# Performance work log

Measured on AMD Instinct MI355X. Metric: run time of the kernel, lower is better.

Reference implementation:

```python
import jax, jax.numpy as jnp
import numpy as np

# Tsit5 (Tsitouras 5(4)) Butcher tableau. 5th-order solution weights b == a7 row (FSAL).
A21 = 0.161
A31, A32 = -0.008480655492356989, 0.335480655492357
A41, A42, A43 = 2.8971530571054935, -6.359448489975075, 4.3622954328695815
A51, A52, A53, A54 = 5.325864828439257, -11.748883564062828, 7.4955393428898365, -0.09249506636175525
A61, A62, A63, A64, A65 = 5.86145544294642, -12.92096931784711, 8.159367898576159, -0.071584973281401, -0.028269050394068383
B1, B2, B3, B4, B5, B6 = 0.09646076681806523, 0.01, 0.4798896504144996, 1.379008574103742, -3.290069515436081, 2.324710524099774

B_TRAJ, D_STATE, D_FORCE, WIDTH = 1024, 256, 256, 512
T0, T1 = 0.0, 1.0
N_STEPS = 60  # fixed step h = DT0*SECOND = 60/3600 = 1/60 hour
H = (T1 - T0) / N_STEPS


def setup_inputs() -> dict:
    key = jax.random.key(0)
    ks = jax.random.split(key, 8)
    din = D_STATE + D_FORCE
    x0 = jax.random.normal(ks[0], (B_TRAJ, D_STATE), jnp.float32)
    u_forced = jax.random.normal(ks[1], (B_TRAJ, D_FORCE), jnp.float32) * 0.1
    W1 = jax.random.normal(ks[2], (WIDTH, din), jnp.float32) / np.sqrt(din)
    b1 = jnp.zeros((WIDTH,), jnp.float32)
    W2 = jax.random.normal(ks[3], (WIDTH, WIDTH), jnp.float32) / np.sqrt(WIDTH)
    b2 = jnp.zeros((WIDTH,), jnp.float32)
    W3 = jax.random.normal(ks[4], (D_STATE, WIDTH), jnp.float32) / np.sqrt(WIDTH)
    b3 = jnp.zeros((D_STATE,), jnp.float32)
    return dict(x0=x0, u_forced=u_forced, W1=W1, b1=b1, W2=W2, b2=b2, W3=W3, b3=b3)


def reference(x0, u_forced, W1, b1, W2, b2, W3, b3):
    # Augmented system: branch 0 = forced trajectory, branch 1 = unforced (zero force).
    # y: (2, B, D_STATE); u: (2, B, D_FORCE)
    y0 = jnp.stack([x0, x0])
    u = jnp.stack([u_forced, jnp.zeros_like(u_forced)])

    def mlp(z):  # z: (2, B, din) -> (2, B, D_STATE); eqx.nn.MLP default relu
        h = jax.nn.relu(jnp.einsum('kbi,oi->kbo', z, W1) + b1)
        h = jax.nn.relu(jnp.einsum('kbi,oi->kbo', h, W2) + b2)
        return jnp.einsum('kbi,oi->kbo', h, W3) + b3

    def f(y):  # ForcedVectorField: mlp(hstack((x, u))) on both branches at once
        return mlp(jnp.concatenate([y, u], axis=-1))

    def tsit5_step(y, _):
        k1 = f(y)
        k2 = f(y + H * (A21 * k1))
        k3 = f(y + H * (A31 * k1 + A32 * k2))
        k4 = f(y + H * (A41 * k1 + A42 * k2 + A43 * k3))
        k5 = f(y + H * (A51 * k1 + A52 * k2 + A53 * k3 + A54 * k4))
        k6 = f(y + H * (A61 * k1 + A62 * k2 + A63 * k3 + A64 * k4 + A65 * k5))
        y_new = y + H * (B1 * k1 + B2 * k2 + B3 * k3 + B4 * k4 + B5 * k5 + B6 * k6)
        return y_new, None

    y_final, _ = jax.lax.scan(jax.checkpoint(tsit5_step), y0, None, length=N_STEPS)
    # (forced_state, unforced_state) at t1, stacked: (2, B, D_STATE)
    return y_final
```

## Files before the change

### kernel.cpp

```cpp
#include <hip/hip_runtime.h>
#include <hip/hip_bf16.h>

typedef short  short8  __attribute__((ext_vector_type(8)));
typedef float  float4v __attribute__((ext_vector_type(4)));

#define NSTEPS 60

constexpr double Hd = 1.0 / 60.0;
constexpr float HA1[1] = { (float)(Hd * 0.161) };
constexpr float HA2[2] = { (float)(Hd * -0.008480655492356989), (float)(Hd * 0.335480655492357) };
constexpr float HA3[3] = { (float)(Hd * 2.8971530571054935), (float)(Hd * -6.359448489975075),
                           (float)(Hd * 4.3622954328695815) };
constexpr float HA4[4] = { (float)(Hd * 5.325864828439257), (float)(Hd * -11.748883564062828),
                           (float)(Hd * 7.4955393428898365), (float)(Hd * -0.09249506636175525) };
constexpr float HA5[5] = { (float)(Hd * 5.86145544294642), (float)(Hd * -12.92096931784711),
                           (float)(Hd * 8.159367898576159), (float)(Hd * -0.071584973281401),
                           (float)(Hd * -0.028269050394068383) };
constexpr float HB6[6] = { (float)(Hd * 0.09646076681806523), (float)(Hd * 0.01),
                           (float)(Hd * 0.4798896504144996), (float)(Hd * 1.379008574103742),
                           (float)(Hd * -3.290069515436081), (float)(Hd * 2.324710524099774) };

__device__ __forceinline__ unsigned short f2bf(float f) {
    union { float f; unsigned u; } v; v.f = f;
    unsigned r = v.u + 0x7fffu + ((v.u >> 16) & 1u);
    return (unsigned short)(r >> 16);
}

__global__ void wconv(const float* __restrict__ W1, const float* __restrict__ W2,
                      const float* __restrict__ W3, unsigned short* __restrict__ ws) {
    int g = blockIdx.x * blockDim.x + threadIdx.x;
    int blk = g >> 6, l = g & 63;
    const float* src;
    if (blk < 256) {
        int b = blk; int nt = b >> 3, ks = b & 7;
        int n = nt * 16 + (l & 15), k = ks * 32 + (l >> 4) * 8;
        src = W1 + n * 512 + k;
    } else if (blk < 768) {
        int b = blk - 256; int nt = b >> 4, ks = b & 15;
        int n = nt * 16 + (l & 15), k = ks * 32 + (l >> 4) * 8;
        src = W2 + n * 512 + k;
    } else {
        int b = blk - 768; int nt = b >> 4, ks = b & 15;
        int n = nt * 16 + (l & 15), k = ks * 32 + (l >> 4) * 8;
        src = W3 + n * 512 + k;
    }
    short8 v;
#pragma unroll
    for (int j = 0; j < 8; ++j) v[j] = (short)f2bf(src[j]);
    *(((short8*)ws) + g) = v;
}

template<int KDIM, int NT>
__device__ __forceinline__ void mfma_block(const unsigned short* __restrict__ lds, int stride,
                                           const short8* __restrict__ wb, int ntg0, int lane,
                                           float4v* acc) {
    const int row  = lane & 15;
    const int koff = (lane >> 4) * 8;
    const int rm   = (row & 7) << 3;
#pragma unroll
    for (int ks = 0; ks < KDIM / 32; ++ks) {
        const int nidx = ks * 32 + koff;
        short8 a = *(const short8*)(lds + row * stride + (nidx ^ rm));
#pragma unroll
        for (int nt = 0; nt < NT; ++nt) {
            short8 b = wb[(size_t)((ntg0 + nt) * (KDIM / 32) + ks) * 64 + lane];
            acc[nt] = __builtin_amdgcn_mfma_f32_16x16x32_bf16(a, b, acc[nt], 0, 0, 0);
        }
    }
}

__global__ void __launch_bounds__(512, 2) odeint(
        const float* __restrict__ x0, const float* __restrict__ uf,
        const float* __restrict__ W1, const float* __restrict__ b1,
        const float* __restrict__ b2, const float* __restrict__ b3,
        const unsigned short* __restrict__ ws, float* __restrict__ out) {
    __shared__ unsigned short xb[16 * 256];
    __shared__ unsigned short hb[16 * 512];
    __shared__ float c1s[8 * 512];
    __shared__ float bias2[512];
    __shared__ float bias3[256];

    const int tid  = threadIdx.x;
    const int wave = tid >> 6, lane = tid & 63;
    const int r0   = blockIdx.x * 8;

    float* utmp = (float*)hb;
    for (int i = tid; i < 8 * 256; i += 512) {
        int row = i >> 8, k = i & 255;
        int g = r0 + row;
        utmp[i] = (g < 1024) ? uf[g * 256 + k] : 0.f;
    }
    bias2[tid] = b2[tid];
    if (tid < 256) bias3[tid] = b3[tid];
    __syncthreads();

    {
        int n = tid;
        float acc8[8];
#pragma unroll
        for (int r = 0; r < 8; ++r) acc8[r] = b1[n];
        const float* wrow = W1 + n * 512 + 256;
        for (int k = 0; k < 256; ++k) {
            float w = wrow[k];
#pragma unroll
            for (int r = 0; r < 8; ++r) acc8[r] += w * utmp[r * 256 + k];
        }
#pragma unroll
        for (int r = 0; r < 8; ++r) c1s[r * 512 + n] = acc8[r];
    }
    __syncthreads();

    float ybr[8];
    float kreg[6][8];
    if (lane < 32) {
#pragma unroll
        for (int e = 0; e < 8; ++e) {
            int nt = e >> 2, r = e & 3;
            int row = (lane >> 4) * 4 + r;
            int n   = (wave * 2 + nt) * 16 + (lane & 15);
            int g   = r0 + row;
            ybr[e] = x0[(g & 1023) * 256 + n];
        }
    }

    const short8* wy1 = (const short8*)ws;
    const short8* w2  = (const short8*)(ws + 131072);
    const short8* w3  = (const short8*)(ws + 393216);

#define DO_STAGE(S, COEF) do {                                                          \
    if (lane < 32) {                                                                    \
        _Pragma("unroll")                                                               \
        for (int e = 0; e < 8; ++e) {                                                   \
            int nt_ = e >> 2, r_ = e & 3;                                               \
            int row_ = (lane >> 4) * 4 + r_;                                            \
            int n_   = (wave * 2 + nt_) * 16 + (lane & 15);                             \
            float v_ = ybr[e];                                                          \
            _Pragma("unroll")                                                           \
            for (int j = 0; j < S; ++j) v_ += COEF[j] * kreg[j][e];                     \
            xb[row_ * 256 + (n_ ^ ((row_ & 7) << 3))] = f2bf(v_);                       \
        }                                                                               \
    }                                                                                   \
    __syncthreads();             \
    {                                      \
        float4v a1[4];                                                                  \
        _Pragma("unroll") for (int q = 0; q < 4; ++q) a1[q] = (float4v){0.f,0.f,0.f,0.f}; \
        mfma_block<256, 4>(xb, 256, wy1, wave * 4, lane, a1);                           \
        if (lane < 32) {                                                                \
            _Pragma("unroll")                                                           \
            for (int nt = 0; nt < 4; ++nt) {                                            \
                int n_g = (wave * 4 + nt) * 16 + (lane & 15);                           \
                _Pragma("unroll")                                                       \
                for (int r = 0; r < 4; ++r) {                                           \
                    int row = (lane >> 4) * 4 + r;                                      \
                    float v = a1[nt][r] + c1s[row * 512 + n_g];                         \
                    v = fmaxf(v, 0.f);                                                  \
                    hb[row * 512 + (n_g ^ ((row & 7) << 3))] = f2bf(v);                 \
                }                                                                       \
            }                                                                           \
        }                                                                               \
    }                                                                                   \
    __syncthreads();                                                   \
    {          \
        float4v a2[4];                                                                  \
        _Pragma("unroll") for (int q = 0; q < 4; ++q) a2[q] = (float4v){0.f,0.f,0.f,0.f}; \
        mfma_block<512, 4>(hb, 512, w2, wave * 4, lane, a2);                            \
        __syncthreads();                                   \
        if (lane < 32) {                                                                \
            _Pragma("unroll")                                                           \
            for (int nt = 0; nt < 4; ++nt) {                                            \
                int n_g = (wave * 4 + nt) * 16 + (lane & 15);                           \
                _Pragma("unroll")                                                       \
                for (int r = 0; r < 4; ++r) {                                           \
                    int row = (lane >> 4) * 4 + r;                                      \
                    float v = a2[nt][r] + bias2[n_g];                                   \
                    v = fmaxf(v, 0.f);                                                  \
                    hb[row * 512 + (n_g ^ ((row & 7) << 3))] = f2bf(v);                 \
                }                                                                       \
            }                                                                           \
        }                                                                               \
    }                                                                                   \
    __syncthreads();                                                   \
    {        \
        float4v a3[2];                                                                  \
        _Pragma("unroll") for (int q = 0; q < 2; ++q) a3[q] = (float4v){0.f,0.f,0.f,0.f}; \
        mfma_block<512, 2>(hb, 512, w3, wave * 2, lane, a3);                            \
        if (lane < 32) {                                                                \
            _Pragma("unroll")                                                           \
            for (int nt = 0; nt < 2; ++nt) {                                            \
                int n_g = (wave * 2 + nt) * 16 + (lane & 15);                           \
                _Pragma("unroll")                                                       \
                for (int r = 0; r < 4; ++r) {                                           \
                    kreg[S][nt * 4 + r] = a3[nt][r] + bias3[n_g];                       \
                }                                                                       \
            }                                                                           \
        }                                                                               \
    }                                                                                   \
} while (0)

    for (int step = 0; step < NSTEPS; ++step) {
        DO_STAGE(0, HA1);
        DO_STAGE(1, HA1);
        DO_STAGE(2, HA2);
        DO_STAGE(3, HA3);
        DO_STAGE(4, HA4);
        DO_STAGE(5, HA5);
        if (lane < 32) {
#pragma unroll
            for (int e = 0; e < 8; ++e) {
                float v = ybr[e];
#pragma unroll
                for (int j = 0; j < 6; ++j) v += HB6[j] * kreg[j][e];
                ybr[e] = v;
            }
        }
    }
#undef DO_STAGE

    if (lane < 32) {
#pragma unroll
        for (int e = 0; e < 8; ++e) {
            int nt = e >> 2, r = e & 3;
            int row = (lane >> 4) * 4 + r;
            int n   = (wave * 2 + nt) * 16 + (lane & 15);
            out[(r0 + row) * 256 + n] = ybr[e];
        }
    }
}

extern "C" void kernel_launch(void* const* d_in, const int* in_sizes, int n_in,
                              void* d_out, int out_size, void* d_ws, size_t ws_size,
                              hipStream_t stream) {
    const float* x0 = (const float*)d_in[0];
    const float* uf = (const float*)d_in[1];
    const float* W1 = (const float*)d_in[2];
    const float* b1 = (const float*)d_in[3];
    const float* W2 = (const float*)d_in[4];
    const float* b2 = (const float*)d_in[5];
    const float* W3 = (const float*)d_in[6];
    const float* b3 = (const float*)d_in[7];
    unsigned short* ws = (unsigned short*)d_ws;

    wconv<<<128, 512, 0, stream>>>(W1, W2, W3, ws);
    odeint<<<256, 512, 0, stream>>>(x0, uf, W1, b1, b2, b3, ws, (float*)d_out);
}
```

Measured before the change: 14.98 ms.

## Process 16 real rows per block and prefetch MFMA operands

Each block now fills all 16 rows of the MFMA tile with real trajectories instead of 8, halving the grid to 128 blocks and removing wasted padded-row compute and duplicated weight streaming. The MFMA inner loop software-prefetches the next A/B fragments, and separate h1/h2 LDS buffers remove one barrier per stage. This trades fewer active blocks (half the CUs idle, one block per CU) and higher LDS use for less redundant work.

```diff
diff --git a/kernel.cpp b/kernel.cpp
--- a/kernel.cpp
+++ b/kernel.cpp
@@ -5,6 +5,9 @@
 typedef float  float4v __attribute__((ext_vector_type(4)));
 
 #define NSTEPS 60
+#define ROWS   16
+#define GRID   128
+#define C1S    518
 
 constexpr double Hd = 1.0 / 60.0;
 constexpr float HA1[1] = { (float)(Hd * 0.161) };
@@ -54,41 +57,59 @@
 __device__ __forceinline__ void mfma_block(const unsigned short* __restrict__ lds, int stride,
                                            const short8* __restrict__ wb, int ntg0, int lane,
                                            float4v* acc) {
+    constexpr int KS = KDIM / 32;
     const int row  = lane & 15;
     const int koff = (lane >> 4) * 8;
     const int rm   = (row & 7) << 3;
-#pragma unroll
-    for (int ks = 0; ks < KDIM / 32; ++ks) {
-        const int nidx = ks * 32 + koff;
-        short8 a = *(const short8*)(lds + row * stride + (nidx ^ rm));
-#pragma unroll
-        for (int nt = 0; nt < NT; ++nt) {
-            short8 b = wb[(size_t)((ntg0 + nt) * (KDIM / 32) + ks) * 64 + lane];
-            acc[nt] = __builtin_amdgcn_mfma_f32_16x16x32_bf16(a, b, acc[nt], 0, 0, 0);
-        }
-    }
-}
-
-__global__ void __launch_bounds__(512, 2) odeint(
+    const short8* wp = wb + (size_t)ntg0 * KS * 64 + lane;
+    short8 a_cur = *(const short8*)(lds + row * stride + (koff ^ rm));
+    short8 b_cur[NT];
+#pragma unroll
+    for (int nt = 0; nt < NT; ++nt) b_cur[nt] = wp[(size_t)nt * KS * 64];
+#pragma unroll
+    for (int ks = 0; ks < KS; ++ks) {
+        short8 a_nxt;
+        short8 b_nxt[NT];
+        if (ks + 1 < KS) {
+            a_nxt = *(const short8*)(lds + row * stride + (((ks + 1) * 32 + koff) ^ rm));
+#pragma unroll
+            for (int nt = 0; nt < NT; ++nt) b_nxt[nt] = wp[((size_t)nt * KS + ks + 1) * 64];
+        }
+#pragma unroll
+        for (int nt = 0; nt < NT; ++nt)
+            acc[nt] = __builtin_amdgcn_mfma_f32_16x16x32_bf16(a_cur, b_cur[nt], acc[nt], 0, 0, 0);
+        a_cur = a_nxt;
+#pragma unroll
+        for (int nt = 0; nt < NT; ++nt) b_cur[nt] = b_nxt[nt];
+    }
+}
+
+__global__ void __launch_bounds__(512, 1) odeint(
         const float* __restrict__ x0, const float* __restrict__ uf,
         const float* __restrict__ W1, const float* __restrict__ b1,
         const float* __restrict__ b2, const float* __restrict__ b3,
         const unsigned short* __restrict__ ws, float* __restrict__ out) {
     __shared__ unsigned short xb[16 * 256];
-    __shared__ unsigned short hb[16 * 512];
-    __shared__ float c1s[8 * 512];
+    __shared__ unsigned short h1[16 * 512];
+    __shared__ unsigned short h2[16 * 512];
+    __shared__ float c1s[16 * C1S];
     __shared__ float bias2[512];
     __shared__ float bias3[256];
 
     const int tid  = threadIdx.x;
     const int wave = tid >> 6, lane = tid & 63;
-    const int r0   = blockIdx.x * 8;
-
-    float* utmp = (float*)hb;
-    for (int i = tid; i < 8 * 256; i += 512) {
-        int row = i >> 8, k = i & 255;
-        int g = r0 + row;
-        utmp[i] = (g < 1024) ? uf[g * 256 + k] : 0.f;
+    const int r0   = blockIdx.x * ROWS;
+
+    float* utmp = (float*)h1;
+    {
+        const bool forced = (r0 < 1024);
+        float4v* ud = (float4v*)utmp;
+        for (int i = tid; i < ROWS * 64; i += 512) {
+            int row = i >> 6, c4 = i & 63;
+            float4v v = {0.f, 0.f, 0.f, 0.f};
+            if (forced) v = *(const float4v*)(uf + (size_t)(r0 + row) * 256 + c4 * 4);
+            ud[i] = v;
+        }
     }
     bias2[tid] = b2[tid];
     if (tid < 256) bias3[tid] = b3[tid];
@@ -96,31 +117,29 @@
 
     {
         int n = tid;
-        float acc8[8];
-#pragma unroll
-        for (int r = 0; r < 8; ++r) acc8[r] = b1[n];
+        float acc16[ROWS];
+        float bb = b1[n];
+#pragma unroll
+        for (int r = 0; r < ROWS; ++r) acc16[r] = bb;
         const float* wrow = W1 + n * 512 + 256;
         for (int k = 0; k < 256; ++k) {
             float w = wrow[k];
 #pragma unroll
-            for (int r = 0; r < 8; ++r) acc8[r] += w * utmp[r * 256 + k];
-        }
-#pragma unroll
-        for (int r = 0; r < 8; ++r) c1s[r * 512 + n] = acc8[r];
+            for (int r = 0; r < ROWS; ++r) acc16[r] += w * utmp[r * 256 + k];
+        }
+#pragma unroll
+        for (int r = 0; r < ROWS; ++r) c1s[r * C1S + n] = acc16[r];
     }
     __syncthreads();
 
     float ybr[8];
     float kreg[6][8];
-    if (lane < 32) {
-#pragma unroll
-        for (int e = 0; e < 8; ++e) {
-            int nt = e >> 2, r = e & 3;
-            int row = (lane >> 4) * 4 + r;
-            int n   = (wave * 2 + nt) * 16 + (lane & 15);
-            int g   = r0 + row;
-            ybr[e] = x0[(g & 1023) * 256 + n];
-        }
+#pragma unroll
+    for (int e = 0; e < 8; ++e) {
+        int nt = e >> 2, r = e & 3;
+        int row = (lane >> 4) * 4 + r;
+        int n   = (wave * 2 + nt) * 16 + (lane & 15);
+        ybr[e] = x0[(size_t)((r0 + row) & 1023) * 256 + n];
     }
 
     const short8* wy1 = (const short8*)ws;
@@ -128,7 +147,7 @@
     const short8* w3  = (const short8*)(ws + 393216);
 
 #define DO_STAGE(S, COEF) do {                                                          \
-    if (lane < 32) {                                                                    \
+    {                \
         _Pragma("unroll")                                                               \
         for (int e = 0; e < 8; ++e) {                                                   \
             int nt_ = e >> 2, r_ = e & 3;                                               \
@@ -140,58 +159,51 @@
             xb[row_ * 256 + (n_ ^ ((row_ & 7) << 3))] = f2bf(v_);                       \
         }                                                                               \
     }                                                                                   \
-    __syncthreads();             \
+    __syncthreads();                                                   \
     {                                      \
         float4v a1[4];                                                                  \
         _Pragma("unroll") for (int q = 0; q < 4; ++q) a1[q] = (float4v){0.f,0.f,0.f,0.f}; \
         mfma_block<256, 4>(xb, 256, wy1, wave * 4, lane, a1);                           \
-        if (lane < 32) {                                                                \
-            _Pragma("unroll")                                                           \
-            for (int nt = 0; nt < 4; ++nt) {                                            \
-                int n_g = (wave * 4 + nt) * 16 + (lane & 15);                           \
-                _Pragma("unroll")                                                       \
-                for (int r = 0; r < 4; ++r) {                                           \
-                    int row = (lane >> 4) * 4 + r;                                      \
-                    float v = a1[nt][r] + c1s[row * 512 + n_g];                         \
-                    v = fmaxf(v, 0.f);                                                  \
-                    hb[row * 512 + (n_g ^ ((row & 7) << 3))] = f2bf(v);                 \
-                }                                                                       \
+        _Pragma("unroll")                                                               \
+        for (int nt = 0; nt < 4; ++nt) {                                                \
+            int n_g = (wave * 4 + nt) * 16 + (lane & 15);                               \
+            _Pragma("unroll")                                                           \
+            for (int r = 0; r < 4; ++r) {                                               \
+                int row = (lane >> 4) * 4 + r;                                          \
+                float v = a1[nt][r] + c1s[row * C1S + n_g];                             \
+                v = fmaxf(v, 0.f);                                                      \
+                h1[row * 512 + (n_g ^ ((row & 7) << 3))] = f2bf(v);                     \
             }                                                                           \
         }                                                                               \
     }                                                                                   \
     __syncthreads();                                                   \
-    {          \
+    {    \
         float4v a2[4];                                                                  \
         _Pragma("unroll") for (int q = 0; q < 4; ++q) a2[q] = (float4v){0.f,0.f,0.f,0.f}; \
-        mfma_block<512, 4>(hb, 512, w2, wave * 4, lane, a2);                            \
-        __syncthreads();                                   \
-        if (lane < 32) {                                                                \
-            _Pragma("unroll")                                                           \
-            for (int nt = 0; nt < 4; ++nt) {                                            \
-                int n_g = (wave * 4 + nt) * 16 + (lane & 15);                           \
-                _Pragma("unroll")                                                       \
-                for (int r = 0; r < 4; ++r) {                                           \
-                    int row = (lane >> 4) * 4 + r;                                      \
-                    float v = a2[nt][r] + bias2[n_g];                                   \
-                    v = fmaxf(v, 0.f);                                                  \
-                    hb[row * 512 + (n_g ^ ((row & 7) << 3))] = f2bf(v);                 \
-                }                                                                       \
+        mfma_block<512, 4>(h1, 512, w2, wave * 4, lane, a2);                            \
+        _Pragma("unroll")                                                               \
+        for (int nt = 0; nt < 4; ++nt) {                                                \
+            int n_g = (wave * 4 + nt) * 16 + (lane & 15);                               \
+            _Pragma("unroll")                                                           \
+            for (int r = 0; r < 4; ++r) {                                               \
+                int row = (lane >> 4) * 4 + r;                                          \
+                float v = a2[nt][r] + bias2[n_g];                                       \
+                v = fmaxf(v, 0.f);                                                      \
+                h2[row * 512 + (n_g ^ ((row & 7) << 3))] = f2bf(v);                     \
             }                                                                           \
         }                                                                               \
     }                                                                                   \
-    __syncthreads();                                                   \
+    __syncthreads();   \
     {        \
         float4v a3[2];                                                                  \
         _Pragma("unroll") for (int q = 0; q < 2; ++q) a3[q] = (float4v){0.f,0.f,0.f,0.f}; \
-        mfma_block<512, 2>(hb, 512, w3, wave * 2, lane, a3);                            \
-        if (lane < 32) {                                                                \
-            _Pragma("unroll")                                                           \
-            for (int nt = 0; nt < 2; ++nt) {                                            \
-                int n_g = (wave * 2 + nt) * 16 + (lane & 15);                           \
-                _Pragma("unroll")                                                       \
-                for (int r = 0; r < 4; ++r) {                                           \
-                    kreg[S][nt * 4 + r] = a3[nt][r] + bias3[n_g];                       \
-                }                                                                       \
+        mfma_block<512, 2>(h2, 512, w3, wave * 2, lane, a3);                            \
+        _Pragma("unroll")                                                               \
+        for (int nt = 0; nt < 2; ++nt) {                                                \
+            int n_g = (wave * 2 + nt) * 16 + (lane & 15);                               \
+            _Pragma("unroll")                                                           \
+            for (int r = 0; r < 4; ++r) {                                               \
+                kreg[S][nt * 4 + r] = a3[nt][r] + bias3[n_g];                           \
             }                                                                           \
         }                                                                               \
     }                                                                                   \
@@ -204,7 +216,7 @@
         DO_STAGE(3, HA3);
         DO_STAGE(4, HA4);
         DO_STAGE(5, HA5);
-        if (lane < 32) {
+        {
 #pragma unroll
             for (int e = 0; e < 8; ++e) {
                 float v = ybr[e];
@@ -216,14 +228,12 @@
     }
 #undef DO_STAGE
 
-    if (lane < 32) {
-#pragma unroll
-        for (int e = 0; e < 8; ++e) {
-            int nt = e >> 2, r = e & 3;
-            int row = (lane >> 4) * 4 + r;
-            int n   = (wave * 2 + nt) * 16 + (lane & 15);
-            out[(r0 + row) * 256 + n] = ybr[e];
-        }
+#pragma unroll
+    for (int e = 0; e < 8; ++e) {
+        int nt = e >> 2, r = e & 3;
+        int row = (lane >> 4) * 4 + r;
+        int n   = (wave * 2 + nt) * 16 + (lane & 15);
+        out[(size_t)(r0 + row) * 256 + n] = ybr[e];
     }
 }
 
@@ -241,5 +251,5 @@
     unsigned short* ws = (unsigned short*)d_ws;
 
     wconv<<<128, 512, 0, stream>>>(W1, W2, W3, ws);
-    odeint<<<256, 512, 0, stream>>>(x0, uf, W1, b1, b2, b3, ws, (float*)d_out);
-}
+    odeint<<<GRID, 512, 0, stream>>>(x0, uf, W1, b1, b2, b3, ws, (float*)d_out);
+}
```

New measurement: 12.02 ms. -19.7%, faster.
